# Performance work log

Measured on AMD Instinct MI355X. Metric: run time of the kernel, lower is better.

Reference implementation:

```python
import jax, jax.numpy as jnp
import numpy as np

B, H, S, D = 4, 16, 2048, 64

def setup_inputs() -> dict:
    key = jax.random.key(0)
    kq, kk, kv = jax.random.split(key, 3)
    q = jax.random.normal(kq, (B, H, S, D), dtype=jnp.float32)
    k = jax.random.normal(kk, (B, H, S, D), dtype=jnp.float32)
    v = jax.random.normal(kv, (B, H, S, D), dtype=jnp.float32)
    return {"q": q, "k": k, "v": v}

def reference(q, k, v):
    # naive unfused attention: scores = QK^T / sqrt(d), softmax, then @ V
    scale = 1.0 / jnp.sqrt(jnp.asarray(q.shape[-1], q.dtype))
    scores = jnp.einsum('bhqd,bhkd->bhqk', q, k) * scale  # [B,H,S,S] materialized
    attn = jax.nn.softmax(scores, axis=-1)
    out = jnp.einsum('bhqk,bhkd->bhqd', attn, v)
    return out
```

## Files before the change

### kernel.cpp

```cpp
#include <hip/hip_runtime.h>


#define S_LEN 2048
#define D_DIM 64
#define N_BH  64
#define QSCALE 0.18033688011112042f

typedef _Float16 half8 __attribute__((ext_vector_type(8)));
typedef _Float16 half4 __attribute__((ext_vector_type(4)));
typedef float floatx16 __attribute__((ext_vector_type(16)));
typedef unsigned int uint4v __attribute__((ext_vector_type(4)));

#define MFMA32(a, b, c) __builtin_amdgcn_mfma_f32_32x32x16_f16((a), (b), (c), 0, 0, 0)

#define GLL16(g, l) __builtin_amdgcn_global_load_lds(                      \
    (const __attribute__((address_space(1))) void*)(g),                    \
    (__attribute__((address_space(3))) void*)(l), 16, 0, 0)

__global__ __launch_bounds__(256) void prep_kernel(
    const float* __restrict__ kg, const float* __restrict__ vg,
    _Float16* __restrict__ kh, _Float16* __restrict__ vt)
{
    __shared__ _Float16 Ls[64 * 64];
    const int tid = threadIdx.x;
    const int bh = blockIdx.y;
    const int sbase = blockIdx.x * 64;
    const size_t gbase = ((size_t)(bh * S_LEN + sbase)) * D_DIM;

#pragma unroll
    for (int i = 0; i < 4; ++i) {
        const int e = i * 1024 + tid * 4;
        const int s = e >> 6, d0 = e & 63;
        const float4 kv = *(const float4*)(kg + gbase + e);
        half4 hk;
        hk[0] = (_Float16)kv.x; hk[1] = (_Float16)kv.y;
        hk[2] = (_Float16)kv.z; hk[3] = (_Float16)kv.w;
        *(half4*)(kh + gbase + e) = hk;
        const float4 vv = *(const float4*)(vg + gbase + e);
        const int sp = (s & ~12) | ((s & 4) << 1) | ((s & 8) >> 1);
        const int base = ((((sp >> 3) ^ ((d0 >> 2) & 7)) << 3) | (sp & 7));
        Ls[(d0 + 0) * 64 + base] = (_Float16)vv.x;
        Ls[(d0 + 1) * 64 + base] = (_Float16)vv.y;
        Ls[(d0 + 2) * 64 + base] = (_Float16)vv.z;
        Ls[(d0 + 3) * 64 + base] = (_Float16)vv.w;
    }
    __syncthreads();
    const int d = tid >> 2, c = tid & 3, sw = (d >> 2) & 7;
    _Float16* dst = vt + ((size_t)(bh * D_DIM + d)) * S_LEN + sbase + c * 16;
    *(half8*)(dst)     = *(const half8*)&Ls[d * 64 + (((2 * c)     ^ sw) << 3)];
    *(half8*)(dst + 8) = *(const half8*)&Ls[d * 64 + (((2 * c + 1) ^ sw) << 3)];
}

__global__ __launch_bounds__(256, 2) void fa_kernel(
    const float* __restrict__ qg, const _Float16* __restrict__ kh,
    const _Float16* __restrict__ vt, float* __restrict__ outg)
{
    __shared__ _Float16 Kl0[64 * 64];
    __shared__ _Float16 Kl1[64 * 64];
    __shared__ _Float16 Vl0[64 * 64];
    __shared__ _Float16 Vl1[64 * 64];

    const int tid = threadIdx.x;
    const int w = tid >> 6;
    const int L = tid & 63;
    const int lq = L & 31;
    const int h = L >> 5;

    const int id = blockIdx.x;
    const int bh   = ((id & 7) << 3) | (id >> 6);
    const int qblk = (id >> 3) & 7;
    const int qrowA = qblk * 256 + w * 32 + lq;

    half8 qbA[4], qbB[4];
    {
        const float* qpA = qg + ((size_t)bh * S_LEN + qrowA) * D_DIM + h * 8;
        const float* qpB = qpA + 128 * D_DIM;
#pragma unroll
        for (int ks = 0; ks < 4; ++ks) {
            const float4 a0 = *(const float4*)(qpA + ks * 16);
            const float4 b0 = *(const float4*)(qpA + ks * 16 + 4);
            const float4 a1 = *(const float4*)(qpB + ks * 16);
            const float4 b1 = *(const float4*)(qpB + ks * 16 + 4);
            qbA[ks][0] = (_Float16)(a0.x * QSCALE);
            qbA[ks][1] = (_Float16)(a0.y * QSCALE);
            qbA[ks][2] = (_Float16)(a0.z * QSCALE);
            qbA[ks][3] = (_Float16)(a0.w * QSCALE);
            qbA[ks][4] = (_Float16)(b0.x * QSCALE);
            qbA[ks][5] = (_Float16)(b0.y * QSCALE);
            qbA[ks][6] = (_Float16)(b0.z * QSCALE);
            qbA[ks][7] = (_Float16)(b0.w * QSCALE);
            qbB[ks][0] = (_Float16)(a1.x * QSCALE);
            qbB[ks][1] = (_Float16)(a1.y * QSCALE);
            qbB[ks][2] = (_Float16)(a1.z * QSCALE);
            qbB[ks][3] = (_Float16)(a1.w * QSCALE);
            qbB[ks][4] = (_Float16)(b1.x * QSCALE);
            qbB[ks][5] = (_Float16)(b1.y * QSCALE);
            qbB[ks][6] = (_Float16)(b1.z * QSCALE);
            qbB[ks][7] = (_Float16)(b1.w * QSCALE);
        }
    }

    floatx16 o0A, o1A, lacA, o0B, o1B, lacB;
#pragma unroll
    for (int r = 0; r < 16; ++r) {
        o0A[r] = 0.f; o1A[r] = 0.f; lacA[r] = 0.f;
        o0B[r] = 0.f; o1B[r] = 0.f; lacB[r] = 0.f;
    }

    half8 ones;
#pragma unroll
    for (int j = 0; j < 8; ++j) ones[j] = (_Float16)1.0f;

    const int rloc = L >> 3, lc = L & 7;
    const int crd = lc ^ rloc;
    const _Float16* kgl = kh + (size_t)bh * S_LEN * D_DIM
                        + (size_t)(w * 16 + rloc) * D_DIM + crd * 8;
    const _Float16* vgl = vt + (size_t)bh * D_DIM * S_LEN
                        + (size_t)(w * 16 + rloc) * S_LEN + crd * 8;
    const int woff = w * 16 * 64;

#define STAGE(KD, VD) do {                                                 \
        GLL16(kgl,                     &KD[woff]);                         \
        GLL16(kgl + (size_t)8 * D_DIM, &KD[woff + 8 * 64]);                \
        GLL16(vgl,                     &VD[woff]);                         \
        GLL16(vgl + (size_t)8 * S_LEN, &VD[woff + 8 * 64]);                \
        kgl += 64 * D_DIM;                                                 \
        vgl += 64;                                                         \
    } while (0)

#define COMPUTE(KB, VB) do {                                               \
                 \
        floatx16 s0A, s1A, s0B, s1B;                                       \
        _Pragma("unroll")                                                  \
        for (int r = 0; r < 16; ++r) {                                     \
            s0A[r] = 0.f; s1A[r] = 0.f; s0B[r] = 0.f; s1B[r] = 0.f;        \
        }                                                                  \
        _Pragma("unroll")                                                  \
        for (int ks = 0; ks < 4; ++ks) {                                   \
            const int sw = (((2 * ks + h) ^ (lq & 7)) << 3);               \
            const half8 ka0 = *(const half8*)&KB[lq * 64 + sw];            \
            const half8 ka1 = *(const half8*)&KB[(32 + lq) * 64 + sw];     \
            s0A = MFMA32(ka0, qbA[ks], s0A);                               \
            s1A = MFMA32(ka1, qbA[ks], s1A);                               \
            s0B = MFMA32(ka0, qbB[ks], s0B);                               \
            s1B = MFMA32(ka1, qbB[ks], s1B);                               \
        }                                                                  \
                           \
        unsigned int pkA0[8], pkA1[8], pkB0[8], pkB1[8];                   \
        _Pragma("unroll")                                                  \
        for (int p = 0; p < 8; ++p) {                                      \
            const auto eA0 = __builtin_amdgcn_cvt_pkrtz(                   \
                __builtin_amdgcn_exp2f(s0A[2 * p]),                        \
                __builtin_amdgcn_exp2f(s0A[2 * p + 1]));                   \
            const auto eA1 = __builtin_amdgcn_cvt_pkrtz(                   \
                __builtin_amdgcn_exp2f(s1A[2 * p]),                        \
                __builtin_amdgcn_exp2f(s1A[2 * p + 1]));                   \
            pkA0[p] = __builtin_bit_cast(unsigned int, eA0);               \
            pkA1[p] = __builtin_bit_cast(unsigned int, eA1);               \
        }                                                                  \
        _Pragma("unroll")                                                  \
        for (int p = 0; p < 8; ++p) {                                      \
            const auto eB0 = __builtin_amdgcn_cvt_pkrtz(                   \
                __builtin_amdgcn_exp2f(s0B[2 * p]),                        \
                __builtin_amdgcn_exp2f(s0B[2 * p + 1]));                   \
            const auto eB1 = __builtin_amdgcn_cvt_pkrtz(                   \
                __builtin_amdgcn_exp2f(s1B[2 * p]),                        \
                __builtin_amdgcn_exp2f(s1B[2 * p + 1]));                   \
            pkB0[p] = __builtin_bit_cast(unsigned int, eB0);               \
            pkB1[p] = __builtin_bit_cast(unsigned int, eB1);               \
        }                                                                  \
            \
        _Pragma("unroll")                                                  \
        for (int mt = 0; mt < 2; ++mt) {                                   \
            const unsigned int* pA = mt ? pkA1 : pkA0;                     \
            const unsigned int* pB = mt ? pkB1 : pkB0;                     \
            const uint4v uA0 = {pA[0], pA[1], pA[2], pA[3]};               \
            const uint4v uA1 = {pA[4], pA[5], pA[6], pA[7]};               \
            const uint4v uB0 = {pB[0], pB[1], pB[2], pB[3]};               \
            const uint4v uB1 = {pB[4], pB[5], pB[6], pB[7]};               \
            const half8 afA0 = __builtin_bit_cast(half8, uA0);             \
            const half8 afA1 = __builtin_bit_cast(half8, uA1);             \
            const half8 afB0 = __builtin_bit_cast(half8, uB0);             \
            const half8 afB1 = __builtin_bit_cast(half8, uB1);             \
            lacA = MFMA32(afA0 + afA1, ones, lacA);                        \
            lacB = MFMA32(afB0 + afB1, ones, lacB);                        \
            _Pragma("unroll")                                              \
            for (int kl = 0; kl < 2; ++kl) {                               \
                const int ksg = mt * 2 + kl;                               \
                const int sw = (((2 * ksg + h) ^ (lq & 7)) << 3);          \
                const half8 vb0 = *(const half8*)&VB[lq * 64 + sw];        \
                const half8 vb1 = *(const half8*)&VB[(32 + lq) * 64 + sw]; \
                const half8 afA = kl ? afA1 : afA0;                        \
                const half8 afB = kl ? afB1 : afB0;                        \
                o0A = MFMA32(afA, vb0, o0A);                               \
                o1A = MFMA32(afA, vb1, o1A);                               \
                o0B = MFMA32(afB, vb0, o0B);                               \
                o1B = MFMA32(afB, vb1, o1B);                               \
            }                                                              \
        }                                                                  \
    } while (0)

    STAGE(Kl0, Vl0);
    __syncthreads();

    for (int it = 0; it < 15; ++it) {
        STAGE(Kl1, Vl1);
        COMPUTE(Kl0, Vl0);
        __syncthreads();
        STAGE(Kl0, Vl0);
        COMPUTE(Kl1, Vl1);
        __syncthreads();
    }
    STAGE(Kl1, Vl1);
    COMPUTE(Kl0, Vl0);
    __syncthreads();
    COMPUTE(Kl1, Vl1);

#undef STAGE
#undef COMPUTE

    float* obA = outg + ((size_t)bh * S_LEN + qblk * 256 + w * 32) * D_DIM;
    float* obB = obA + (size_t)128 * D_DIM;
#pragma unroll
    for (int reg = 0; reg < 16; ++reg) {
        const int q = (reg & 3) + 8 * (reg >> 2) + 4 * h;
        const float invA = 1.0f / lacA[reg];
        const float invB = 1.0f / lacB[reg];
        obA[(size_t)q * D_DIM + lq]      = o0A[reg] * invA;
        obA[(size_t)q * D_DIM + 32 + lq] = o1A[reg] * invA;
        obB[(size_t)q * D_DIM + lq]      = o0B[reg] * invB;
        obB[(size_t)q * D_DIM + 32 + lq] = o1B[reg] * invB;
    }
}

extern "C" void kernel_launch(void* const* d_in, const int* in_sizes, int n_in,
                              void* d_out, int out_size, void* d_ws, size_t ws_size,
                              hipStream_t stream) {
    const float* q = (const float*)d_in[0];
    const float* k = (const float*)d_in[1];
    const float* v = (const float*)d_in[2];
    float* out = (float*)d_out;
    (void)in_sizes; (void)n_in; (void)out_size; (void)ws_size;

    _Float16* kh = (_Float16*)d_ws;
    _Float16* vt = kh + (size_t)N_BH * S_LEN * D_DIM;

    prep_kernel<<<dim3(S_LEN / 64, N_BH), dim3(256), 0, stream>>>(k, v, kh, vt);
    fa_kernel<<<dim3(512), dim3(256), 0, stream>>>(q, kh, vt, out);
}
```

Baseline: 203.0 us.

## Interleave B-half exp2 with A-half PV MFMAs and widen prep tiles

```diff
diff --git a/kernel.cpp b/kernel.cpp
--- a/kernel.cpp
+++ b/kernel.cpp
@@ -21,34 +21,46 @@
     const float* __restrict__ kg, const float* __restrict__ vg,
     _Float16* __restrict__ kh, _Float16* __restrict__ vt)
 {
-    __shared__ _Float16 Ls[64 * 64];
+    __shared__ _Float16 Ls[64 * 132];
     const int tid = threadIdx.x;
     const int bh = blockIdx.y;
-    const int sbase = blockIdx.x * 64;
+    const int sbase = blockIdx.x * 128;
     const size_t gbase = ((size_t)(bh * S_LEN + sbase)) * D_DIM;
 
 #pragma unroll
-    for (int i = 0; i < 4; ++i) {
+    for (int i = 0; i < 8; ++i) {
         const int e = i * 1024 + tid * 4;
-        const int s = e >> 6, d0 = e & 63;
         const float4 kv = *(const float4*)(kg + gbase + e);
         half4 hk;
         hk[0] = (_Float16)kv.x; hk[1] = (_Float16)kv.y;
         hk[2] = (_Float16)kv.z; hk[3] = (_Float16)kv.w;
         *(half4*)(kh + gbase + e) = hk;
+    }
+#pragma unroll
+    for (int i = 0; i < 8; ++i) {
+        const int e = i * 1024 + tid * 4;
+        const int s = e >> 6, d0 = e & 63;
         const float4 vv = *(const float4*)(vg + gbase + e);
         const int sp = (s & ~12) | ((s & 4) << 1) | ((s & 8) >> 1);
-        const int base = ((((sp >> 3) ^ ((d0 >> 2) & 7)) << 3) | (sp & 7));
-        Ls[(d0 + 0) * 64 + base] = (_Float16)vv.x;
-        Ls[(d0 + 1) * 64 + base] = (_Float16)vv.y;
-        Ls[(d0 + 2) * 64 + base] = (_Float16)vv.z;
-        Ls[(d0 + 3) * 64 + base] = (_Float16)vv.w;
+        Ls[(d0 + 0) * 132 + sp] = (_Float16)vv.x;
+        Ls[(d0 + 1) * 132 + sp] = (_Float16)vv.y;
+        Ls[(d0 + 2) * 132 + sp] = (_Float16)vv.z;
+        Ls[(d0 + 3) * 132 + sp] = (_Float16)vv.w;
     }
     __syncthreads();
-    const int d = tid >> 2, c = tid & 3, sw = (d >> 2) & 7;
-    _Float16* dst = vt + ((size_t)(bh * D_DIM + d)) * S_LEN + sbase + c * 16;
-    *(half8*)(dst)     = *(const half8*)&Ls[d * 64 + (((2 * c)     ^ sw) << 3)];
-    *(half8*)(dst + 8) = *(const half8*)&Ls[d * 64 + (((2 * c + 1) ^ sw) << 3)];
+    const int w = tid >> 6, L = tid & 63;
+    const int dr = L >> 4;
+    const int c  = L & 15;
+#pragma unroll
+    for (int k = 0; k < 4; ++k) {
+        const int d = w * 16 + k * 4 + dr;
+        const half4 lo = *(const half4*)&Ls[d * 132 + c * 8];
+        const half4 hi = *(const half4*)&Ls[d * 132 + c * 8 + 4];
+        half8 o;
+        o[0] = lo[0]; o[1] = lo[1]; o[2] = lo[2]; o[3] = lo[3];
+        o[4] = hi[0]; o[5] = hi[1]; o[6] = hi[2]; o[7] = hi[3];
+        *(half8*)(vt + ((size_t)(bh * D_DIM + d)) * S_LEN + sbase + c * 8) = o;
+    }
 }
 
 __global__ __launch_bounds__(256, 2) void fa_kernel(
@@ -128,8 +140,19 @@
         vgl += 64;                                                         \
     } while (0)
 
+#define EXPB(p) do {                                                       \
+        const auto eB0 = __builtin_amdgcn_cvt_pkrtz(                       \
+            __builtin_amdgcn_exp2f(s0B[2 * (p)]),                          \
+            __builtin_amdgcn_exp2f(s0B[2 * (p) + 1]));                     \
+        const auto eB1 = __builtin_amdgcn_cvt_pkrtz(                       \
+            __builtin_amdgcn_exp2f(s1B[2 * (p)]),                          \
+            __builtin_amdgcn_exp2f(s1B[2 * (p) + 1]));                     \
+        pkB0[p] = __builtin_bit_cast(unsigned int, eB0);                   \
+        pkB1[p] = __builtin_bit_cast(unsigned int, eB1);                   \
+    } while (0)
+
 #define COMPUTE(KB, VB) do {                                               \
-                 \
+              \
         floatx16 s0A, s1A, s0B, s1B;                                       \
         _Pragma("unroll")                                                  \
         for (int r = 0; r < 16; ++r) {                                     \
@@ -145,7 +168,15 @@
             s0B = MFMA32(ka0, qbB[ks], s0B);                               \
             s1B = MFMA32(ka1, qbB[ks], s1B);                               \
         }                                                                  \
-                           \
+           \
+        half8 vbl[4], vbh[4];                                              \
+        _Pragma("unroll")                                                  \
+        for (int ksg = 0; ksg < 4; ++ksg) {                                \
+            const int sw = (((2 * ksg + h) ^ (lq & 7)) << 3);              \
+            vbl[ksg] = *(const half8*)&VB[lq * 64 + sw];                   \
+            vbh[ksg] = *(const half8*)&VB[(32 + lq) * 64 + sw];            \
+        }                                                                  \
+                      \
         unsigned int pkA0[8], pkA1[8], pkB0[8], pkB1[8];                   \
         _Pragma("unroll")                                                  \
         for (int p = 0; p < 8; ++p) {                                      \
@@ -158,46 +189,51 @@
             pkA0[p] = __builtin_bit_cast(unsigned int, eA0);               \
             pkA1[p] = __builtin_bit_cast(unsigned int, eA1);               \
         }                                                                  \
-        _Pragma("unroll")                                                  \
-        for (int p = 0; p < 8; ++p) {                                      \
-            const auto eB0 = __builtin_amdgcn_cvt_pkrtz(                   \
-                __builtin_amdgcn_exp2f(s0B[2 * p]),                        \
-                __builtin_amdgcn_exp2f(s0B[2 * p + 1]));                   \
-            const auto eB1 = __builtin_amdgcn_cvt_pkrtz(                   \
-                __builtin_amdgcn_exp2f(s1B[2 * p]),                        \
-                __builtin_amdgcn_exp2f(s1B[2 * p + 1]));                   \
-            pkB0[p] = __builtin_bit_cast(unsigned int, eB0);               \
-            pkB1[p] = __builtin_bit_cast(unsigned int, eB1);               \
-        }                                                                  \
-            \
-        _Pragma("unroll")                                                  \
-        for (int mt = 0; mt < 2; ++mt) {                                   \
-            const unsigned int* pA = mt ? pkA1 : pkA0;                     \
-            const unsigned int* pB = mt ? pkB1 : pkB0;                     \
-            const uint4v uA0 = {pA[0], pA[1], pA[2], pA[3]};               \
-            const uint4v uA1 = {pA[4], pA[5], pA[6], pA[7]};               \
-            const uint4v uB0 = {pB[0], pB[1], pB[2], pB[3]};               \
-            const uint4v uB1 = {pB[4], pB[5], pB[6], pB[7]};               \
-            const half8 afA0 = __builtin_bit_cast(half8, uA0);             \
-            const half8 afA1 = __builtin_bit_cast(half8, uA1);             \
-            const half8 afB0 = __builtin_bit_cast(half8, uB0);             \
-            const half8 afB1 = __builtin_bit_cast(half8, uB1);             \
-            lacA = MFMA32(afA0 + afA1, ones, lacA);                        \
-            lacB = MFMA32(afB0 + afB1, ones, lacB);                        \
-            _Pragma("unroll")                                              \
-            for (int kl = 0; kl < 2; ++kl) {                               \
-                const int ksg = mt * 2 + kl;                               \
-                const int sw = (((2 * ksg + h) ^ (lq & 7)) << 3);          \
-                const half8 vb0 = *(const half8*)&VB[lq * 64 + sw];        \
-                const half8 vb1 = *(const half8*)&VB[(32 + lq) * 64 + sw]; \
-                const half8 afA = kl ? afA1 : afA0;                        \
-                const half8 afB = kl ? afB1 : afB0;                        \
-                o0A = MFMA32(afA, vb0, o0A);                               \
-                o1A = MFMA32(afA, vb1, o1A);                               \
-                o0B = MFMA32(afB, vb0, o0B);                               \
-                o1B = MFMA32(afB, vb1, o1B);                               \
-            }                                                              \
-        }                                                                  \
+        const uint4v uA00 = {pkA0[0], pkA0[1], pkA0[2], pkA0[3]};          \
+        const uint4v uA01 = {pkA0[4], pkA0[5], pkA0[6], pkA0[7]};          \
+        const uint4v uA10 = {pkA1[0], pkA1[1], pkA1[2], pkA1[3]};          \
+        const uint4v uA11 = {pkA1[4], pkA1[5], pkA1[6], pkA1[7]};          \
+        const half8 afA00 = __builtin_bit_cast(half8, uA00);               \
+        const half8 afA01 = __builtin_bit_cast(half8, uA01);               \
+        const half8 afA10 = __builtin_bit_cast(half8, uA10);               \
+        const half8 afA11 = __builtin_bit_cast(half8, uA11);               \
+                      \
+        lacA = MFMA32(afA00 + afA01, ones, lacA);                          \
+        EXPB(0); EXPB(1);                                                  \
+        o0A = MFMA32(afA00, vbl[0], o0A);                                  \
+        EXPB(2);                                                           \
+        o1A = MFMA32(afA00, vbh[0], o1A);                                  \
+        EXPB(3);                                                           \
+        o0A = MFMA32(afA01, vbl[1], o0A);                                  \
+        EXPB(4);                                                           \
+        o1A = MFMA32(afA01, vbh[1], o1A);                                  \
+        EXPB(5);                                                           \
+        lacA = MFMA32(afA10 + afA11, ones, lacA);                          \
+        EXPB(6);                                                           \
+        o0A = MFMA32(afA10, vbl[2], o0A);                                  \
+        EXPB(7);                                                           \
+        o1A = MFMA32(afA10, vbh[2], o1A);                                  \
+        o0A = MFMA32(afA11, vbl[3], o0A);                                  \
+        o1A = MFMA32(afA11, vbh[3], o1A);                                  \
+                                                        \
+        const uint4v uB00 = {pkB0[0], pkB0[1], pkB0[2], pkB0[3]};          \
+        const uint4v uB01 = {pkB0[4], pkB0[5], pkB0[6], pkB0[7]};          \
+        const uint4v uB10 = {pkB1[0], pkB1[1], pkB1[2], pkB1[3]};          \
+        const uint4v uB11 = {pkB1[4], pkB1[5], pkB1[6], pkB1[7]};          \
+        const half8 afB00 = __builtin_bit_cast(half8, uB00);               \
+        const half8 afB01 = __builtin_bit_cast(half8, uB01);               \
+        const half8 afB10 = __builtin_bit_cast(half8, uB10);               \
+        const half8 afB11 = __builtin_bit_cast(half8, uB11);               \
+        lacB = MFMA32(afB00 + afB01, ones, lacB);                          \
+        o0B = MFMA32(afB00, vbl[0], o0B);                                  \
+        o1B = MFMA32(afB00, vbh[0], o1B);                                  \
+        o0B = MFMA32(afB01, vbl[1], o0B);                                  \
+        o1B = MFMA32(afB01, vbh[1], o1B);                                  \
+        lacB = MFMA32(afB10 + afB11, ones, lacB);                          \
+        o0B = MFMA32(afB10, vbl[2], o0B);                                  \
+        o1B = MFMA32(afB10, vbh[2], o1B);                                  \
+        o0B = MFMA32(afB11, vbl[3], o0B);                                  \
+        o1B = MFMA32(afB11, vbh[3], o1B);                                  \
     } while (0)
 
     STAGE(Kl0, Vl0);
@@ -218,6 +254,7 @@
 
 #undef STAGE
 #undef COMPUTE
+#undef EXPB
 
     float* obA = outg + ((size_t)bh * S_LEN + qblk * 256 + w * 32) * D_DIM;
     float* obB = obA + (size_t)128 * D_DIM;
@@ -245,6 +282,6 @@
     _Float16* kh = (_Float16*)d_ws;
     _Float16* vt = kh + (size_t)N_BH * S_LEN * D_DIM;
 
-    prep_kernel<<<dim3(S_LEN / 64, N_BH), dim3(256), 0, stream>>>(k, v, kh, vt);
+    prep_kernel<<<dim3(S_LEN / 128, N_BH), dim3(256), 0, stream>>>(k, v, kh, vt);
     fa_kernel<<<dim3(512), dim3(256), 0, stream>>>(q, kh, vt, out);
 }
```

Result: slower. 231.0 us (+13.8%).
